# Optimization experiments

Measured on AMD Instinct MI355X. Metric: run time of the kernel, lower is better.

## Reference

```python
import jax, jax.numpy as jnp
import numpy as np

THRESHOLD = 10.0  # degrees, PlanetaryGraphConstruction default


def _norm_adj(lon):
    # lon: [B, P] longitudes in degrees
    diff = jnp.abs(lon[:, :, None] - lon[:, None, :]) % 360.0
    dist = jnp.minimum(diff, 360.0 - diff)            # circular angular distance, diag = 0
    mask = (dist < THRESHOLD).astype(lon.dtype)       # distance edges (diag included: 0 < 10)
    P = lon.shape[1]
    A = mask + jnp.eye(P, dtype=lon.dtype)            # GCNConv add_self_loops appends another self loop
    deg = A.sum(-1)
    dinv = jax.lax.rsqrt(jnp.maximum(deg, 1e-12))
    return A * dinv[:, :, None] * dinv[:, None, :]    # D^-1/2 (A+I) D^-1/2, [B, P, P]


def setup_inputs() -> dict:
    key = jax.random.key(0)
    ks = jax.random.split(key, 10)
    B, P, Din, H, Dout = 65536, 12, 32, 128, 3
    L = 3
    x = jax.random.uniform(ks[0], (B, P, Din), dtype=jnp.float32) * 360.0  # col 0 = longitude in degrees
    s = 0.02
    return {
        "x": x,
        "W_in": jax.random.normal(ks[1], (Din, H), jnp.float32) * s,
        "b_in": jnp.zeros((H,), jnp.float32),
        "W_gcn": jax.random.normal(ks[2], (L, H, H), jnp.float32) * s,
        "b_gcn": jnp.zeros((L, H), jnp.float32),
        "W_out1": jax.random.normal(ks[3], (H, H // 2), jnp.float32) * s,
        "b_out1": jnp.zeros((H // 2,), jnp.float32),
        "W_out2": jax.random.normal(ks[4], (H // 2, Dout), jnp.float32) * s,
        "b_out2": jnp.zeros((Dout,), jnp.float32),
    }


def reference(x, W_in, b_in, W_gcn, b_gcn, W_out1, b_out1, W_out2, b_out2):
    # x: [B, P, Din]
    Ahat = _norm_adj(x[:, :, 0])                      # [B, P, P] normalized adjacency
    h = x @ W_in + b_in                               # input projection, [B, P, H]
    for l in range(W_gcn.shape[0]):                   # GCN layers (dropout = identity in eval)
        h = jnp.einsum('bij,bjh->bih', Ahat, h @ W_gcn[l]) + b_gcn[l]
        h = jax.nn.relu(h)
    g = h.mean(axis=1)                                # mean pool over planets, [B, H]
    g = jax.nn.relu(g @ W_out1 + b_out1)
    return g @ W_out2 + b_out2                        # [B, Dout]
```

## Files before the change

kernel.cpp:

```cpp
#include <hip/hip_runtime.h>


typedef _Float16 half4v __attribute__((ext_vector_type(4)));
typedef _Float16 half8v __attribute__((ext_vector_type(8)));
typedef float    float4v __attribute__((ext_vector_type(4)));

constexpr int PP = 12, DIN = 32, H = 128, HO = 64, DOUT = 3, NL = 3;
constexpr int NB = 8;
constexpr int AP2 = 72;
constexpr int GTS = 136;

constexpr int WS_WG = 4096, WS_W1 = 53248, WS_TOT = 61440;

__global__ __launch_bounds__(256)
void prep_weights(const float* __restrict__ W_in, const float* __restrict__ W_gcn,
                  const float* __restrict__ W_out1, _Float16* __restrict__ ws)
{
    int e = blockIdx.x * 256 + threadIdx.x;
    if (e < WS_WG) {
        int n = e >> 5, k = e & 31;
        ws[e] = (_Float16)W_in[k * H + n];
    } else if (e < WS_W1) {
        int e2 = e - WS_WG;
        int l = e2 >> 14, r = e2 & 16383, n = r >> 7, k = r & 127;
        ws[e] = (_Float16)W_gcn[l * (H * H) + k * H + n];
    } else if (e < WS_TOT) {
        int e3 = e - WS_W1;
        int o = e3 >> 7, k = e3 & 127;
        ws[e] = (_Float16)W_out1[k * HO + o];
    }
}

__device__ inline half4v pk4(float a, float b, float c, float d) {
    half4v r; r[0] = (_Float16)a; r[1] = (_Float16)b; r[2] = (_Float16)c; r[3] = (_Float16)d;
    return r;
}

__global__ __launch_bounds__(256, 4)
void gnn_mfma(const float* __restrict__ x,
              const float* __restrict__ b_in,
              const float* __restrict__ b_gcn,
              const float* __restrict__ b_out1,
              const float* __restrict__ W_out2,
              const float* __restrict__ b_out2,
              const _Float16* __restrict__ ws,
              float* __restrict__ out)
{
    __shared__ __align__(16) _Float16 hf[2][12][512];
    __shared__ __align__(16) _Float16 Am[2 * 48 * AP2];
    _Float16* gTT = &hf[0][0][0];
    float*    psf = (float*)&hf[1][0][0];

    const int tid  = threadIdx.x;
    const int lane = tid & 63, wave = tid >> 6;
    const int q = lane >> 4, qm = lane & 15;
    const int hh = lane >> 5, l32 = lane & 31;
    const int b0 = blockIdx.x * NB;
    const float* xblk = x + (size_t)b0 * (PP * DIN);
    const _Float16* WgT = ws + WS_WG;

    float lon_own = 0.f;
    if (l32 < PP) lon_own = xblk[(hh * 48 + wave * PP + l32) * DIN];
    float4 xa[3], xb[3];
    #pragma unroll
    for (int nt = 0; nt < 3; ++nt) {
        const float* p = xblk + (16 * nt + qm) * DIN + 8 * q;
        xa[nt] = *(const float4*)p;
        xb[nt] = *(const float4*)(p + 4);
    }

    {
        float lonj[PP];
        #pragma unroll
        for (int j = 0; j < PP; ++j) lonj[j] = __shfl(lon_own, j, 32);
        float deg = 1.0f;
        #pragma unroll
        for (int j = 0; j < PP; ++j) {
            float d = fabsf(lon_own - lonj[j]);
            d = fminf(d, 360.0f - d);
            deg += (d < 10.0f) ? 1.0f : 0.0f;
        }
        float dinv_own = rsqrtf(fmaxf(deg, 1e-12f));
        float dj[PP];
        #pragma unroll
        for (int j = 0; j < PP; ++j) dj[j] = __shfl(dinv_own, j, 32);

        if (l32 < PP) {
            _Float16* Ar = Am + (hh * 48 + wave * PP + l32) * AP2;
            half8v z = {0, 0, 0, 0, 0, 0, 0, 0};
            #pragma unroll
            for (int c = 0; c < 48; c += 8) *(half8v*)&Ar[c] = z;
            _Float16 vals[PP];
            #pragma unroll
            for (int j = 0; j < PP; ++j) {
                float d = fabsf(lon_own - lonj[j]);
                d = fminf(d, 360.0f - d);
                float a = (d < 10.0f) ? 1.0f : 0.0f;
                if (j == l32) a += 1.0f;
                vals[j] = (_Float16)(a * dinv_own * dj[j]);
            }
            #pragma unroll
            for (int t4 = 0; t4 < 3; ++t4) {
                half4v v;
                v[0] = vals[4 * t4]; v[1] = vals[4 * t4 + 1];
                v[2] = vals[4 * t4 + 2]; v[3] = vals[4 * t4 + 3];
                *(half4v*)&Ar[wave * PP + 4 * t4] = v;
            }
        }
    }

    half8v bxA[3];
    #pragma unroll
    for (int nt = 0; nt < 3; ++nt) {
        half8v h;
        h[0] = (_Float16)xa[nt].x; h[1] = (_Float16)xa[nt].y;
        h[2] = (_Float16)xa[nt].z; h[3] = (_Float16)xa[nt].w;
        h[4] = (_Float16)xb[nt].x; h[5] = (_Float16)xb[nt].y;
        h[6] = (_Float16)xb[nt].z; h[7] = (_Float16)xb[nt].w;
        bxA[nt] = h;
    }
    #pragma unroll
    for (int nt = 0; nt < 3; ++nt) {
        const float* p = xblk + (48 + 16 * nt + qm) * DIN + 8 * q;
        xa[nt] = *(const float4*)p;
        xb[nt] = *(const float4*)(p + 4);
    }

    {
        const int m0 = 32 * wave, m1 = 32 * wave + 16;
        half8v aw0 = *(const half8v*)&ws[(m0 + qm) * DIN + 8 * q];
        half8v aw1 = *(const half8v*)&ws[(m1 + qm) * DIN + 8 * q];
        float4 bi0 = *(const float4*)&b_in[m0 + 4 * q];
        float4 bi1 = *(const float4*)&b_in[m1 + 4 * q];
        const int ho0 = (qm + 16 * ((q >> 1) & 3)) * 8 + (q & 1) * 4;
        const int ho1 = (qm + 16 * ((2 + (q >> 1)) & 3)) * 8 + (q & 1) * 4;
        #pragma unroll
        for (int nt = 0; nt < 3; ++nt) {
            float4v c0 = {0.f, 0.f, 0.f, 0.f}, c1 = {0.f, 0.f, 0.f, 0.f};
            c0 = __builtin_amdgcn_mfma_f32_16x16x32_f16(aw0, bxA[nt], c0, 0, 0, 0);
            c1 = __builtin_amdgcn_mfma_f32_16x16x32_f16(aw1, bxA[nt], c1, 0, 0, 0);
            *(half4v*)&hf[0][nt * 4 + wave][ho0] =
                pk4(c0[0] + bi0.x, c0[1] + bi0.y, c0[2] + bi0.z, c0[3] + bi0.w);
            *(half4v*)&hf[0][nt * 4 + wave][ho1] =
                pk4(c1[0] + bi1.x, c1[1] + bi1.y, c1[2] + bi1.z, c1[3] + bi1.w);
        }
        half8v bxB[3];
        #pragma unroll
        for (int nt = 0; nt < 3; ++nt) {
            half8v h;
            h[0] = (_Float16)xa[nt].x; h[1] = (_Float16)xa[nt].y;
            h[2] = (_Float16)xa[nt].z; h[3] = (_Float16)xa[nt].w;
            h[4] = (_Float16)xb[nt].x; h[5] = (_Float16)xb[nt].y;
            h[6] = (_Float16)xb[nt].z; h[7] = (_Float16)xb[nt].w;
            bxB[nt] = h;
        }
        #pragma unroll
        for (int nt = 0; nt < 3; ++nt) {
            float4v c0 = {0.f, 0.f, 0.f, 0.f}, c1 = {0.f, 0.f, 0.f, 0.f};
            c0 = __builtin_amdgcn_mfma_f32_16x16x32_f16(aw0, bxB[nt], c0, 0, 0, 0);
            c1 = __builtin_amdgcn_mfma_f32_16x16x32_f16(aw1, bxB[nt], c1, 0, 0, 0);
            *(half4v*)&hf[1][nt * 4 + wave][ho0] =
                pk4(c0[0] + bi0.x, c0[1] + bi0.y, c0[2] + bi0.z, c0[3] + bi0.w);
            *(half4v*)&hf[1][nt * 4 + wave][ho1] =
                pk4(c1[0] + bi1.x, c1[1] + bi1.y, c1[2] + bi1.z, c1[3] + bi1.w);
        }
    }

    half8v bw[2][4];
    #pragma unroll
    for (int n2 = 0; n2 < 2; ++n2)
        #pragma unroll
        for (int kt = 0; kt < 4; ++kt)
            bw[n2][kt] = *(const half8v*)&WgT[(32 * wave + 16 * n2 + qm) * H + 32 * kt + 8 * q];

    __syncthreads();

    #pragma unroll
    for (int l = 0; l < NL; ++l) {
        half4v ah[2][3][2];
        #pragma unroll
        for (int h = 0; h < 2; ++h) {
            float4v c[3][2];
            #pragma unroll
            for (int mt = 0; mt < 3; ++mt) {
                c[mt][0] = (float4v){0.f, 0.f, 0.f, 0.f};
                c[mt][1] = (float4v){0.f, 0.f, 0.f, 0.f};
            }
            #pragma unroll
            for (int kt = 0; kt < 4; ++kt)
                #pragma unroll
                for (int mt = 0; mt < 3; ++mt) {
                    half8v a = *(const half8v*)&hf[h][mt * 4 + kt][lane * 8];
                    c[mt][0] = __builtin_amdgcn_mfma_f32_16x16x32_f16(a, bw[0][kt], c[mt][0], 0, 0, 0);
                    c[mt][1] = __builtin_amdgcn_mfma_f32_16x16x32_f16(a, bw[1][kt], c[mt][1], 0, 0, 0);
                }
            #pragma unroll
            for (int mt = 0; mt < 3; ++mt)
                #pragma unroll
                for (int n2 = 0; n2 < 2; ++n2)
                    ah[h][mt][n2] = pk4(c[mt][n2][0], c[mt][n2][1], c[mt][n2][2], c[mt][n2][3]);
        }

        if (l < 2) {
            const float4 bg0 = *(const float4*)&b_gcn[l * H + 32 * wave + 4 * q];
            const float4 bg1 = *(const float4*)&b_gcn[l * H + 32 * wave + 16 + 4 * q];
            __syncthreads();

            {
                const _Float16* Wn = WgT + (l + 1) * (H * H);
                #pragma unroll
                for (int n2 = 0; n2 < 2; ++n2)
                    #pragma unroll
                    for (int kt = 0; kt < 4; ++kt)
                        bw[n2][kt] = *(const half8v*)&Wn[(32 * wave + 16 * n2 + qm) * H + 32 * kt + 8 * q];
            }

            #pragma unroll
            for (int h = 0; h < 2; ++h) {
                const _Float16* Ah = Am + h * 48 * AP2;
                const half4v bA00 = *(const half4v*)&Ah[qm * AP2 + 4 * q];
                const half4v bA10 = *(const half4v*)&Ah[qm * AP2 + 16 + 4 * q];
                const half4v bA01 = *(const half4v*)&Ah[(16 + qm) * AP2 + 4 * q];
                const half4v bA11 = *(const half4v*)&Ah[(16 + qm) * AP2 + 16 + 4 * q];
                const half4v bA21 = *(const half4v*)&Ah[(16 + qm) * AP2 + 32 + 4 * q];
                const half4v bA12 = *(const half4v*)&Ah[(32 + qm) * AP2 + 16 + 4 * q];
                const half4v bA22 = *(const half4v*)&Ah[(32 + qm) * AP2 + 32 + 4 * q];
                #pragma unroll
                for (int n2 = 0; n2 < 2; ++n2) {
                    const float4 bg = n2 ? bg1 : bg0;
                    const int hoff = (qm + 16 * ((2 * n2 + (q >> 1)) & 3)) * 8 + (q & 1) * 4;

                    float4v d0 = {0.f, 0.f, 0.f, 0.f};
                    d0 = __builtin_amdgcn_mfma_f32_16x16x16f16(ah[h][0][n2], bA00, d0, 0, 0, 0);
                    d0 = __builtin_amdgcn_mfma_f32_16x16x16f16(ah[h][1][n2], bA10, d0, 0, 0, 0);
                    *(half4v*)&hf[h][0 * 4 + wave][hoff] =
                        pk4(fmaxf(d0[0] + bg.x, 0.f), fmaxf(d0[1] + bg.y, 0.f),
                            fmaxf(d0[2] + bg.z, 0.f), fmaxf(d0[3] + bg.w, 0.f));

                    float4v d1 = {0.f, 0.f, 0.f, 0.f};
                    d1 = __builtin_amdgcn_mfma_f32_16x16x16f16(ah[h][0][n2], bA01, d1, 0, 0, 0);
                    d1 = __builtin_amdgcn_mfma_f32_16x16x16f16(ah[h][1][n2], bA11, d1, 0, 0, 0);
                    d1 = __builtin_amdgcn_mfma_f32_16x16x16f16(ah[h][2][n2], bA21, d1, 0, 0, 0);
                    *(half4v*)&hf[h][1 * 4 + wave][hoff] =
                        pk4(fmaxf(d1[0] + bg.x, 0.f), fmaxf(d1[1] + bg.y, 0.f),
                            fmaxf(d1[2] + bg.z, 0.f), fmaxf(d1[3] + bg.w, 0.f));

                    float4v d2 = {0.f, 0.f, 0.f, 0.f};
                    d2 = __builtin_amdgcn_mfma_f32_16x16x16f16(ah[h][1][n2], bA12, d2, 0, 0, 0);
                    d2 = __builtin_amdgcn_mfma_f32_16x16x16f16(ah[h][2][n2], bA22, d2, 0, 0, 0);
                    *(half4v*)&hf[h][2 * 4 + wave][hoff] =
                        pk4(fmaxf(d2[0] + bg.x, 0.f), fmaxf(d2[1] + bg.y, 0.f),
                            fmaxf(d2[2] + bg.z, 0.f), fmaxf(d2[3] + bg.w, 0.f));
                }
            }
            __syncthreads();
        } else {
            __syncthreads();
            const float bgc0 = b_gcn[2 * H + 32 * wave + qm];
            const float bgc1 = b_gcn[2 * H + 32 * wave + 16 + qm];
            #pragma unroll
            for (int h = 0; h < 2; ++h) {
                const _Float16* Ah = Am + h * 48 * AP2;
                const half4v bA00 = *(const half4v*)&Ah[qm * AP2 + 4 * q];
                const half4v bA10 = *(const half4v*)&Ah[qm * AP2 + 16 + 4 * q];
                const half4v bA01 = *(const half4v*)&Ah[(16 + qm) * AP2 + 4 * q];
                const half4v bA11 = *(const half4v*)&Ah[(16 + qm) * AP2 + 16 + 4 * q];
                const half4v bA21 = *(const half4v*)&Ah[(16 + qm) * AP2 + 32 + 4 * q];
                const half4v bA12 = *(const half4v*)&Ah[(32 + qm) * AP2 + 16 + 4 * q];
                const half4v bA22 = *(const half4v*)&Ah[(32 + qm) * AP2 + 32 + 4 * q];
                float s[3][2];
                #pragma unroll
                for (int n2 = 0; n2 < 2; ++n2) {
                    const float bgc = n2 ? bgc1 : bgc0;
                    float4v d;
                    d = (float4v){0.f, 0.f, 0.f, 0.f};
                    d = __builtin_amdgcn_mfma_f32_16x16x16f16(bA00, ah[h][0][n2], d, 0, 0, 0);
                    d = __builtin_amdgcn_mfma_f32_16x16x16f16(bA10, ah[h][1][n2], d, 0, 0, 0);
                    s[0][n2] = fmaxf(d[0] + bgc, 0.f) + fmaxf(d[1] + bgc, 0.f)
                             + fmaxf(d[2] + bgc, 0.f) + fmaxf(d[3] + bgc, 0.f);
                    d = (float4v){0.f, 0.f, 0.f, 0.f};
                    d = __builtin_amdgcn_mfma_f32_16x16x16f16(bA01, ah[h][0][n2], d, 0, 0, 0);
                    d = __builtin_amdgcn_mfma_f32_16x16x16f16(bA11, ah[h][1][n2], d, 0, 0, 0);
                    d = __builtin_amdgcn_mfma_f32_16x16x16f16(bA21, ah[h][2][n2], d, 0, 0, 0);
                    s[1][n2] = fmaxf(d[0] + bgc, 0.f) + fmaxf(d[1] + bgc, 0.f)
                             + fmaxf(d[2] + bgc, 0.f) + fmaxf(d[3] + bgc, 0.f);
                    d = (float4v){0.f, 0.f, 0.f, 0.f};
                    d = __builtin_amdgcn_mfma_f32_16x16x16f16(bA12, ah[h][1][n2], d, 0, 0, 0);
                    d = __builtin_amdgcn_mfma_f32_16x16x16f16(bA22, ah[h][2][n2], d, 0, 0, 0);
                    s[2][n2] = fmaxf(d[0] + bgc, 0.f) + fmaxf(d[1] + bgc, 0.f)
                             + fmaxf(d[2] + bgc, 0.f) + fmaxf(d[3] + bgc, 0.f);
                }
                #pragma unroll
                for (int n2 = 0; n2 < 2; ++n2) {
                    float g4[4];
                    g4[0] = (q <= 2) ? s[0][n2] : 0.f;
                    g4[1] = (q == 3) ? s[0][n2] : ((q <= 1) ? s[1][n2] : 0.f);
                    g4[2] = (q >= 2) ? s[1][n2] : ((q == 0) ? s[2][n2] : 0.f);
                    g4[3] = (q >= 1) ? s[2][n2] : 0.f;
                    #pragma unroll
                    for (int b = 0; b < 4; ++b) {
                        float v = g4[b];
                        v += __shfl_xor(v, 16, 64);
                        v += __shfl_xor(v, 32, 64);
                        if (q == 0)
                            gTT[(4 * h + b) * GTS + 32 * wave + 16 * n2 + qm] =
                                (_Float16)(v * (1.0f / 12.0f));
                    }
                }
            }
            __syncthreads();
        }
    }

    float4v acc = {0.f, 0.f, 0.f, 0.f};
    #pragma unroll
    for (int kt = 0; kt < 4; ++kt) {
        half8v aW = *(const half8v*)&ws[WS_W1 + (16 * wave + qm) * H + 32 * kt + 8 * q];
        half8v bG = *(const half8v*)&gTT[qm * GTS + 32 * kt + 8 * q];
        acc = __builtin_amdgcn_mfma_f32_16x16x32_f16(aW, bG, acc, 0, 0, 0);
    }
    const float4 b1v = *(const float4*)&b_out1[16 * wave + 4 * q];
    float o1v[4];
    o1v[0] = fmaxf(acc[0] + b1v.x, 0.f);
    o1v[1] = fmaxf(acc[1] + b1v.y, 0.f);
    o1v[2] = fmaxf(acc[2] + b1v.z, 0.f);
    o1v[3] = fmaxf(acc[3] + b1v.w, 0.f);
    const float* w2p = W_out2 + (16 * wave + 4 * q) * DOUT;
    const float4 w2a = *(const float4*)(w2p);
    const float4 w2b = *(const float4*)(w2p + 4);
    const float4 w2c = *(const float4*)(w2p + 8);
    float p0 = o1v[0] * w2a.x + o1v[1] * w2a.w + o1v[2] * w2b.z + o1v[3] * w2c.y;
    float p1 = o1v[0] * w2a.y + o1v[1] * w2b.x + o1v[2] * w2b.w + o1v[3] * w2c.z;
    float p2 = o1v[0] * w2a.z + o1v[1] * w2b.y + o1v[2] * w2c.x + o1v[3] * w2c.w;
    p0 += __shfl_xor(p0, 16, 64); p0 += __shfl_xor(p0, 32, 64);
    p1 += __shfl_xor(p1, 16, 64); p1 += __shfl_xor(p1, 32, 64);
    p2 += __shfl_xor(p2, 16, 64); p2 += __shfl_xor(p2, 32, 64);
    if (q == 0 && qm < NB) {
        psf[wave * (NB * DOUT) + qm * DOUT + 0] = p0;
        psf[wave * (NB * DOUT) + qm * DOUT + 1] = p1;
        psf[wave * (NB * DOUT) + qm * DOUT + 2] = p2;
    }
    __syncthreads();
    if (tid < NB * DOUT) {
        const int b = tid / 3, d = tid - 3 * b;
        const float ssum = psf[b * 3 + d] + psf[24 + b * 3 + d]
                         + psf[48 + b * 3 + d] + psf[72 + b * 3 + d] + b_out2[d];
        out[(size_t)(b0 + b) * DOUT + d] = ssum;
    }
}

extern "C" void kernel_launch(void* const* d_in, const int* in_sizes, int n_in,
                              void* d_out, int out_size, void* d_ws, size_t ws_size,
                              hipStream_t stream) {
    const float* x      = (const float*)d_in[0];
    const float* W_in   = (const float*)d_in[1];
    const float* b_in   = (const float*)d_in[2];
    const float* W_gcn  = (const float*)d_in[3];
    const float* b_gcn  = (const float*)d_in[4];
    const float* W_out1 = (const float*)d_in[5];
    const float* b_out1 = (const float*)d_in[6];
    const float* W_out2 = (const float*)d_in[7];
    const float* b_out2 = (const float*)d_in[8];
    float* outp         = (float*)d_out;
    _Float16* wsh       = (_Float16*)d_ws;

    const int B = in_sizes[0] / (PP * DIN);

    hipLaunchKernelGGL(prep_weights, dim3((WS_TOT + 255) / 256), dim3(256), 0, stream,
                       W_in, W_gcn, W_out1, wsh);
    hipLaunchKernelGGL(gnn_mfma, dim3(B / NB), dim3(256), 0, stream,
                       x, b_in, b_gcn, b_out1, W_out2, b_out2, wsh, outp);
}
```

Baseline: 292.5 us.

## Keep adjacency fragments in registers, alias LDS, fold biases into MFMA accumulators

The normalized adjacency fragments are loaded from shared memory into registers once, right after they are built. The separate adjacency LDS buffer is then dropped by aliasing it onto the activation buffer, with extra barriers to keep that safe, and the launch bound is raised to 5 blocks per CU. Biases are used as the initial MFMA accumulator values instead of being added afterwards. The aim is to cut LDS footprint and repeated LDS reads so occupancy can rise, at the cost of 14 more live half4 registers per thread under a tighter register cap, which could cause spills.

```diff
diff --git a/kernel.cpp b/kernel.cpp
--- a/kernel.cpp
+++ b/kernel.cpp
@@ -36,7 +36,7 @@
     return r;
 }
 
-__global__ __launch_bounds__(256, 4)
+__global__ __launch_bounds__(256, 5)
 void gnn_mfma(const float* __restrict__ x,
               const float* __restrict__ b_in,
               const float* __restrict__ b_gcn,
@@ -47,7 +47,7 @@
               float* __restrict__ out)
 {
     __shared__ __align__(16) _Float16 hf[2][12][512];
-    __shared__ __align__(16) _Float16 Am[2 * 48 * AP2];
+    _Float16* Am  = &hf[0][0][0];
     _Float16* gTT = &hf[0][0][0];
     float*    psf = (float*)&hf[1][0][0];
 
@@ -108,6 +108,21 @@
             }
         }
     }
+    __syncthreads();
+
+    half4v bAf[2][7];
+    #pragma unroll
+    for (int h = 0; h < 2; ++h) {
+        const _Float16* Ah = Am + h * 48 * AP2;
+        bAf[h][0] = *(const half4v*)&Ah[qm * AP2 + 4 * q];
+        bAf[h][1] = *(const half4v*)&Ah[qm * AP2 + 16 + 4 * q];
+        bAf[h][2] = *(const half4v*)&Ah[(16 + qm) * AP2 + 4 * q];
+        bAf[h][3] = *(const half4v*)&Ah[(16 + qm) * AP2 + 16 + 4 * q];
+        bAf[h][4] = *(const half4v*)&Ah[(16 + qm) * AP2 + 32 + 4 * q];
+        bAf[h][5] = *(const half4v*)&Ah[(32 + qm) * AP2 + 16 + 4 * q];
+        bAf[h][6] = *(const half4v*)&Ah[(32 + qm) * AP2 + 32 + 4 * q];
+    }
+    __syncthreads();
 
     half8v bxA[3];
     #pragma unroll
@@ -132,17 +147,17 @@
         half8v aw1 = *(const half8v*)&ws[(m1 + qm) * DIN + 8 * q];
         float4 bi0 = *(const float4*)&b_in[m0 + 4 * q];
         float4 bi1 = *(const float4*)&b_in[m1 + 4 * q];
+        const float4v ci0 = {bi0.x, bi0.y, bi0.z, bi0.w};
+        const float4v ci1 = {bi1.x, bi1.y, bi1.z, bi1.w};
         const int ho0 = (qm + 16 * ((q >> 1) & 3)) * 8 + (q & 1) * 4;
         const int ho1 = (qm + 16 * ((2 + (q >> 1)) & 3)) * 8 + (q & 1) * 4;
         #pragma unroll
         for (int nt = 0; nt < 3; ++nt) {
-            float4v c0 = {0.f, 0.f, 0.f, 0.f}, c1 = {0.f, 0.f, 0.f, 0.f};
+            float4v c0 = ci0, c1 = ci1;
             c0 = __builtin_amdgcn_mfma_f32_16x16x32_f16(aw0, bxA[nt], c0, 0, 0, 0);
             c1 = __builtin_amdgcn_mfma_f32_16x16x32_f16(aw1, bxA[nt], c1, 0, 0, 0);
-            *(half4v*)&hf[0][nt * 4 + wave][ho0] =
-                pk4(c0[0] + bi0.x, c0[1] + bi0.y, c0[2] + bi0.z, c0[3] + bi0.w);
-            *(half4v*)&hf[0][nt * 4 + wave][ho1] =
-                pk4(c1[0] + bi1.x, c1[1] + bi1.y, c1[2] + bi1.z, c1[3] + bi1.w);
+            *(half4v*)&hf[0][nt * 4 + wave][ho0] = pk4(c0[0], c0[1], c0[2], c0[3]);
+            *(half4v*)&hf[0][nt * 4 + wave][ho1] = pk4(c1[0], c1[1], c1[2], c1[3]);
         }
         half8v bxB[3];
         #pragma unroll
@@ -156,13 +171,11 @@
         }
         #pragma unroll
         for (int nt = 0; nt < 3; ++nt) {
-            float4v c0 = {0.f, 0.f, 0.f, 0.f}, c1 = {0.f, 0.f, 0.f, 0.f};
+            float4v c0 = ci0, c1 = ci1;
             c0 = __builtin_amdgcn_mfma_f32_16x16x32_f16(aw0, bxB[nt], c0, 0, 0, 0);
             c1 = __builtin_amdgcn_mfma_f32_16x16x32_f16(aw1, bxB[nt], c1, 0, 0, 0);
-            *(half4v*)&hf[1][nt * 4 + wave][ho0] =
-                pk4(c0[0] + bi0.x, c0[1] + bi0.y, c0[2] + bi0.z, c0[3] + bi0.w);
-            *(half4v*)&hf[1][nt * 4 + wave][ho1] =
-                pk4(c1[0] + bi1.x, c1[1] + bi1.y, c1[2] + bi1.z, c1[3] + bi1.w);
+            *(half4v*)&hf[1][nt * 4 + wave][ho0] = pk4(c0[0], c0[1], c0[2], c0[3]);
+            *(half4v*)&hf[1][nt * 4 + wave][ho1] = pk4(c1[0], c1[1], c1[2], c1[3]);
         }
     }
 
@@ -217,40 +230,33 @@
 
             #pragma unroll
             for (int h = 0; h < 2; ++h) {
-                const _Float16* Ah = Am + h * 48 * AP2;
-                const half4v bA00 = *(const half4v*)&Ah[qm * AP2 + 4 * q];
-                const half4v bA10 = *(const half4v*)&Ah[qm * AP2 + 16 + 4 * q];
-                const half4v bA01 = *(const half4v*)&Ah[(16 + qm) * AP2 + 4 * q];
-                const half4v bA11 = *(const half4v*)&Ah[(16 + qm) * AP2 + 16 + 4 * q];
-                const half4v bA21 = *(const half4v*)&Ah[(16 + qm) * AP2 + 32 + 4 * q];
-                const half4v bA12 = *(const half4v*)&Ah[(32 + qm) * AP2 + 16 + 4 * q];
-                const half4v bA22 = *(const half4v*)&Ah[(32 + qm) * AP2 + 32 + 4 * q];
                 #pragma unroll
                 for (int n2 = 0; n2 < 2; ++n2) {
                     const float4 bg = n2 ? bg1 : bg0;
+                    const float4v di = {bg.x, bg.y, bg.z, bg.w};
                     const int hoff = (qm + 16 * ((2 * n2 + (q >> 1)) & 3)) * 8 + (q & 1) * 4;
 
-                    float4v d0 = {0.f, 0.f, 0.f, 0.f};
-                    d0 = __builtin_amdgcn_mfma_f32_16x16x16f16(ah[h][0][n2], bA00, d0, 0, 0, 0);
-                    d0 = __builtin_amdgcn_mfma_f32_16x16x16f16(ah[h][1][n2], bA10, d0, 0, 0, 0);
+                    float4v d0 = di;
+                    d0 = __builtin_amdgcn_mfma_f32_16x16x16f16(ah[h][0][n2], bAf[h][0], d0, 0, 0, 0);
+                    d0 = __builtin_amdgcn_mfma_f32_16x16x16f16(ah[h][1][n2], bAf[h][1], d0, 0, 0, 0);
                     *(half4v*)&hf[h][0 * 4 + wave][hoff] =
-                        pk4(fmaxf(d0[0] + bg.x, 0.f), fmaxf(d0[1] + bg.y, 0.f),
-                            fmaxf(d0[2] + bg.z, 0.f), fmaxf(d0[3] + bg.w, 0.f));
-
-                    float4v d1 = {0.f, 0.f, 0.f, 0.f};
-                    d1 = __builtin_amdgcn_mfma_f32_16x16x16f16(ah[h][0][n2], bA01, d1, 0, 0, 0);
-                    d1 = __builtin_amdgcn_mfma_f32_16x16x16f16(ah[h][1][n2], bA11, d1, 0, 0, 0);
-                    d1 = __builtin_amdgcn_mfma_f32_16x16x16f16(ah[h][2][n2], bA21, d1, 0, 0, 0);
+                        pk4(fmaxf(d0[0], 0.f), fmaxf(d0[1], 0.f),
+                            fmaxf(d0[2], 0.f), fmaxf(d0[3], 0.f));
+
+                    float4v d1 = di;
+                    d1 = __builtin_amdgcn_mfma_f32_16x16x16f16(ah[h][0][n2], bAf[h][2], d1, 0, 0, 0);
+                    d1 = __builtin_amdgcn_mfma_f32_16x16x16f16(ah[h][1][n2], bAf[h][3], d1, 0, 0, 0);
+                    d1 = __builtin_amdgcn_mfma_f32_16x16x16f16(ah[h][2][n2], bAf[h][4], d1, 0, 0, 0);
                     *(half4v*)&hf[h][1 * 4 + wave][hoff] =
-                        pk4(fmaxf(d1[0] + bg.x, 0.f), fmaxf(d1[1] + bg.y, 0.f),
-                            fmaxf(d1[2] + bg.z, 0.f), fmaxf(d1[3] + bg.w, 0.f));
-
-                    float4v d2 = {0.f, 0.f, 0.f, 0.f};
-                    d2 = __builtin_amdgcn_mfma_f32_16x16x16f16(ah[h][1][n2], bA12, d2, 0, 0, 0);
-                    d2 = __builtin_amdgcn_mfma_f32_16x16x16f16(ah[h][2][n2], bA22, d2, 0, 0, 0);
+                        pk4(fmaxf(d1[0], 0.f), fmaxf(d1[1], 0.f),
+                            fmaxf(d1[2], 0.f), fmaxf(d1[3], 0.f));
+
+                    float4v d2 = di;
+                    d2 = __builtin_amdgcn_mfma_f32_16x16x16f16(ah[h][1][n2], bAf[h][5], d2, 0, 0, 0);
+                    d2 = __builtin_amdgcn_mfma_f32_16x16x16f16(ah[h][2][n2], bAf[h][6], d2, 0, 0, 0);
                     *(half4v*)&hf[h][2 * 4 + wave][hoff] =
-                        pk4(fmaxf(d2[0] + bg.x, 0.f), fmaxf(d2[1] + bg.y, 0.f),
-                            fmaxf(d2[2] + bg.z, 0.f), fmaxf(d2[3] + bg.w, 0.f));
+                        pk4(fmaxf(d2[0], 0.f), fmaxf(d2[1], 0.f),
+                            fmaxf(d2[2], 0.f), fmaxf(d2[3], 0.f));
                 }
             }
             __syncthreads();
@@ -260,35 +266,28 @@
             const float bgc1 = b_gcn[2 * H + 32 * wave + 16 + qm];
             #pragma unroll
             for (int h = 0; h < 2; ++h) {
-                const _Float16* Ah = Am + h * 48 * AP2;
-                const half4v bA00 = *(const half4v*)&Ah[qm * AP2 + 4 * q];
-                const half4v bA10 = *(const half4v*)&Ah[qm * AP2 + 16 + 4 * q];
-                const half4v bA01 = *(const half4v*)&Ah[(16 + qm) * AP2 + 4 * q];
-                const half4v bA11 = *(const half4v*)&Ah[(16 + qm) * AP2 + 16 + 4 * q];
-                const half4v bA21 = *(const half4v*)&Ah[(16 + qm) * AP2 + 32 + 4 * q];
-                const half4v bA12 = *(const half4v*)&Ah[(32 + qm) * AP2 + 16 + 4 * q];
-                const half4v bA22 = *(const half4v*)&Ah[(32 + qm) * AP2 + 32 + 4 * q];
                 float s[3][2];
                 #pragma unroll
                 for (int n2 = 0; n2 < 2; ++n2) {
                     const float bgc = n2 ? bgc1 : bgc0;
+                    const float4v di = {bgc, bgc, bgc, bgc};
                     float4v d;
-                    d = (float4v){0.f, 0.f, 0.f, 0.f};
-                    d = __builtin_amdgcn_mfma_f32_16x16x16f16(bA00, ah[h][0][n2], d, 0, 0, 0);
-                    d = __builtin_amdgcn_mfma_f32_16x16x16f16(bA10, ah[h][1][n2], d, 0, 0, 0);
-                    s[0][n2] = fmaxf(d[0] + bgc, 0.f) + fmaxf(d[1] + bgc, 0.f)
-                             + fmaxf(d[2] + bgc, 0.f) + fmaxf(d[3] + bgc, 0.f);
-                    d = (float4v){0.f, 0.f, 0.f, 0.f};
-                    d = __builtin_amdgcn_mfma_f32_16x16x16f16(bA01, ah[h][0][n2], d, 0, 0, 0);
-                    d = __builtin_amdgcn_mfma_f32_16x16x16f16(bA11, ah[h][1][n2], d, 0, 0, 0);
-                    d = __builtin_amdgcn_mfma_f32_16x16x16f16(bA21, ah[h][2][n2], d, 0, 0, 0);
-                    s[1][n2] = fmaxf(d[0] + bgc, 0.f) + fmaxf(d[1] + bgc, 0.f)
-                             + fmaxf(d[2] + bgc, 0.f) + fmaxf(d[3] + bgc, 0.f);
-                    d = (float4v){0.f, 0.f, 0.f, 0.f};
-                    d = __builtin_amdgcn_mfma_f32_16x16x16f16(bA12, ah[h][1][n2], d, 0, 0, 0);
-                    d = __builtin_amdgcn_mfma_f32_16x16x16f16(bA22, ah[h][2][n2], d, 0, 0, 0);
-                    s[2][n2] = fmaxf(d[0] + bgc, 0.f) + fmaxf(d[1] + bgc, 0.f)
-                             + fmaxf(d[2] + bgc, 0.f) + fmaxf(d[3] + bgc, 0.f);
+                    d = di;
+                    d = __builtin_amdgcn_mfma_f32_16x16x16f16(bAf[h][0], ah[h][0][n2], d, 0, 0, 0);
+                    d = __builtin_amdgcn_mfma_f32_16x16x16f16(bAf[h][1], ah[h][1][n2], d, 0, 0, 0);
+                    s[0][n2] = fmaxf(d[0], 0.f) + fmaxf(d[1], 0.f)
+                             + fmaxf(d[2], 0.f) + fmaxf(d[3], 0.f);
+                    d = di;
+                    d = __builtin_amdgcn_mfma_f32_16x16x16f16(bAf[h][2], ah[h][0][n2], d, 0, 0, 0);
+                    d = __builtin_amdgcn_mfma_f32_16x16x16f16(bAf[h][3], ah[h][1][n2], d, 0, 0, 0);
+                    d = __builtin_amdgcn_mfma_f32_16x16x16f16(bAf[h][4], ah[h][2][n2], d, 0, 0, 0);
+                    s[1][n2] = fmaxf(d[0], 0.f) + fmaxf(d[1], 0.f)
+                             + fmaxf(d[2], 0.f) + fmaxf(d[3], 0.f);
+                    d = di;
+                    d = __builtin_amdgcn_mfma_f32_16x16x16f16(bAf[h][5], ah[h][1][n2], d, 0, 0, 0);
+                    d = __builtin_amdgcn_mfma_f32_16x16x16f16(bAf[h][6], ah[h][2][n2], d, 0, 0, 0);
+                    s[2][n2] = fmaxf(d[0], 0.f) + fmaxf(d[1], 0.f)
+                             + fmaxf(d[2], 0.f) + fmaxf(d[3], 0.f);
                 }
                 #pragma unroll
                 for (int n2 = 0; n2 < 2; ++n2) {
@@ -312,19 +311,19 @@
         }
     }
 
-    float4v acc = {0.f, 0.f, 0.f, 0.f};
+    const float4 b1v = *(const float4*)&b_out1[16 * wave + 4 * q];
+    float4v acc = {b1v.x, b1v.y, b1v.z, b1v.w};
     #pragma unroll
     for (int kt = 0; kt < 4; ++kt) {
         half8v aW = *(const half8v*)&ws[WS_W1 + (16 * wave + qm) * H + 32 * kt + 8 * q];
         half8v bG = *(const half8v*)&gTT[qm * GTS + 32 * kt + 8 * q];
         acc = __builtin_amdgcn_mfma_f32_16x16x32_f16(aW, bG, acc, 0, 0, 0);
     }
-    const float4 b1v = *(const float4*)&b_out1[16 * wave + 4 * q];
     float o1v[4];
-    o1v[0] = fmaxf(acc[0] + b1v.x, 0.f);
-    o1v[1] = fmaxf(acc[1] + b1v.y, 0.f);
-    o1v[2] = fmaxf(acc[2] + b1v.z, 0.f);
-    o1v[3] = fmaxf(acc[3] + b1v.w, 0.f);
+    o1v[0] = fmaxf(acc[0], 0.f);
+    o1v[1] = fmaxf(acc[1], 0.f);
+    o1v[2] = fmaxf(acc[2], 0.f);
+    o1v[3] = fmaxf(acc[3], 0.f);
     const float* w2p = W_out2 + (16 * wave + 4 * q) * DOUT;
     const float4 w2a = *(const float4*)(w2p);
     const float4 w2b = *(const float4*)(w2p + 4);
```

After: 379.0 us. 1.3x slower.
